# Optimization experiments

Hardware: AMD Instinct MI355X
Metric: run time of the kernel (lower is better)

## Reference

```python
import jax, jax.numpy as jnp
import numpy as np

N = 64      # SSM state size (hidden_size)
H = 1024    # channels
L = 2048    # sequence length
BATCH = 8


def setup_inputs() -> dict:
    key = jax.random.key(0)
    ks = jax.random.split(key, 12)
    s = 1.0 / np.sqrt(N)
    n = jnp.arange(N, dtype=jnp.float32)
    return {
        "r": jax.random.normal(ks[0], (BATCH, L, H), dtype=jnp.float32),
        "B_re": jax.random.normal(ks[1], (N,), dtype=jnp.float32) * s,
        "B_im": jax.random.normal(ks[2], (N,), dtype=jnp.float32) * s,
        "C_re": jax.random.normal(ks[3], (H, N), dtype=jnp.float32) * s,
        "C_im": jax.random.normal(ks[4], (H, N), dtype=jnp.float32) * s,
        "P_re": jax.random.normal(ks[5], (N,), dtype=jnp.float32) * s,
        "P_im": jax.random.normal(ks[6], (N,), dtype=jnp.float32) * s,
        "Q_re": jax.random.normal(ks[7], (N,), dtype=jnp.float32) * s,
        "Q_im": jax.random.normal(ks[8], (N,), dtype=jnp.float32) * s,
        # HiPPO-LegS-like diagonal: negative real part for stability, imag ~ pi*n
        "diag_re": -0.5 * jnp.ones((N,), dtype=jnp.float32),
        "diag_im": jnp.pi * (n - N / 2.0),
        "step": jnp.array([1e-3], dtype=jnp.float32),
        "D": jnp.zeros((1,), dtype=jnp.float32),
    }


def _dplr_kernel(Bc, Cc, Pc, Qc, Lam, step, seq_len):
    # Standard S4 DPLR generating function evaluated at roots of unity,
    # then inverse FFT -> real convolution kernel K_c of shape (H, L).
    z = jnp.exp(-2j * jnp.pi * jnp.arange(seq_len) / seq_len).astype(jnp.complex64)  # (L,)
    g = (2.0 / step) * (1.0 - z) / (1.0 + z)                                          # (L,)
    cden = 1.0 / (g[:, None] - Lam[None, :])                                          # (L,N) Cauchy denom
    k00 = jnp.einsum('hn,ln->hl', Cc * Bc, cden)   # (H,L)
    k01 = jnp.einsum('hn,ln->hl', Cc * Pc, cden)   # (H,L)
    k10 = jnp.einsum('n,ln->l', Qc * Bc, cden)     # (L,)
    k11 = jnp.einsum('n,ln->l', Qc * Pc, cden)     # (L,)
    at_roots = (2.0 / (1.0 + z)) * (k00 - k01 * (k10 / (1.0 + k11)))  # (H,L)
    return jnp.fft.ifft(at_roots, axis=-1).real


def reference(r, B_re, B_im, C_re, C_im, P_re, P_im, Q_re, Q_im,
              diag_re, diag_im, step, D):
    step_c = jnp.maximum(step[0], 1e-6)
    Bc = B_re + 1j * B_im
    Cc = C_re + 1j * C_im
    Pc = P_re + 1j * P_im
    Qc = Q_re + 1j * Q_im
    Lam = diag_re + 1j * diag_im
    seq_len = r.shape[1]
    K = _dplr_kernel(Bc, Cc, Pc, Qc, Lam, step_c, seq_len)  # (H, L)
    # causal FFT convolution along the sequence axis
    nfft = 2 * seq_len
    Kf = jnp.fft.rfft(K, n=nfft, axis=-1)            # (H, nfft//2+1)
    uf = jnp.fft.rfft(r, n=nfft, axis=1)             # (B, nfft//2+1, H)
    h1 = jnp.fft.irfft(uf * Kf.T[None], n=nfft, axis=1)[:, :seq_len]  # (B,L,H)
    y1 = h1 + D[0] * r
    return jax.nn.gelu(y1, approximate=False)
```

## Files before the change

kernel.cpp:

```cpp
#include <hip/hip_runtime.h>
#include <math.h>

#define SSM_N 64
#define SSM_H 1024
#define SSM_L 2048
#define SSM_B 8
#define FFTN 2048
#define NT 256

#define PSWZ(a) ((a) ^ (((a) >> 4) & 15))

typedef float f2 __attribute__((ext_vector_type(2)));
static __device__ __forceinline__ f2 mkf2(float a, float b){ f2 v; v.x = a; v.y = b; return v; }

static __device__ __forceinline__ f2 cmul(f2 a, f2 b){
  return mkf2(-a.y, a.y) * mkf2(b.y, b.x) + mkf2(a.x, a.x) * b;
}
static __device__ __forceinline__ f2 cconj(f2 a){ return mkf2(a.x, -a.y); }

template<bool INV> static __device__ __forceinline__ f2 mul_mi(f2 a){
  return INV ? mkf2(-a.y, a.x) : mkf2(a.y, -a.x);
}
template<bool INV> static __device__ __forceinline__ f2 mul_w81(f2 a){
  const float r = 0.70710678118654752440f;
  return INV ? (r * mkf2(a.x - a.y, a.y + a.x)) : (r * mkf2(a.x + a.y, a.y - a.x));
}
template<bool INV> static __device__ __forceinline__ f2 mul_w83(f2 a){
  const float r = 0.70710678118654752440f;
  return INV ? (r * mkf2(-(a.x + a.y), a.x - a.y)) : (r * mkf2(a.y - a.x, -(a.x + a.y)));
}

#define W8C0 1.f
#define W8S0 0.f
#define W8C1 0.92387953251f
#define W8S1 (-0.38268343236f)
#define W8C2 0.70710678119f
#define W8S2 (-0.70710678119f)
#define W8C3 0.38268343236f
#define W8S3 (-0.92387953251f)
#define W8C4 0.f
#define W8S4 (-1.f)
#define W8C5 (-0.38268343236f)
#define W8S5 (-0.92387953251f)
#define W8C6 (-0.70710678119f)
#define W8S6 (-0.70710678119f)
#define W8C7 (-0.92387953251f)
#define W8S7 (-0.38268343236f)

template<bool INV>
static __device__ __forceinline__ void bfly8_store(f2* __restrict__ dst, const f2* __restrict__ tw,
                                                   f2* x, int j, int base, int S)
{
  f2 t0=x[0]+x[4], t4=x[0]-x[4];
  f2 t1=x[1]+x[5], t5=x[1]-x[5];
  f2 t2=x[2]+x[6], t6=x[2]-x[6];
  f2 t3=x[3]+x[7], t7=x[3]-x[7];
  f2 b0=t0+t2, b2=t0-t2, b1=t1+t3, b3=t1-t3;
  f2 mb3 = mul_mi<INV>(b3);
  f2 y0=b0+b1, y4=b0-b1, y2=b2+mb3, y6=b2-mb3;
  f2 v1 = mul_w81<INV>(t5), v2 = mul_mi<INV>(t6), v3 = mul_w83<INV>(t7);
  f2 a0=t4+v2, a2=t4-v2, a1=v1+v3, a3=v1-v3;
  f2 ma3 = mul_mi<INV>(a3);
  f2 y1=a0+a1, y5=a0-a1, y3=a2+ma3, y7=a2-ma3;
  f2 w1 = tw[j];
  if (INV) w1.y = -w1.y;
  f2 w2 = cmul(w1,w1);
  f2 w3 = cmul(w2,w1);
  f2 w4 = cmul(w2,w2);
  f2 w5 = cmul(w3,w2);
  f2 w6 = cmul(w3,w3);
  f2 w7 = cmul(w4,w3);
  dst[PSWZ(base)]     = y0;
  dst[PSWZ(base+S)]   = cmul(y1,w1);
  dst[PSWZ(base+2*S)] = cmul(y2,w2);
  dst[PSWZ(base+3*S)] = cmul(y3,w3);
  dst[PSWZ(base+4*S)] = cmul(y4,w4);
  dst[PSWZ(base+5*S)] = cmul(y5,w5);
  dst[PSWZ(base+6*S)] = cmul(y6,w6);
  dst[PSWZ(base+7*S)] = cmul(y7,w7);
}

template<bool INV, bool ZTOP>
static __device__ __forceinline__ void stage8_first(const f2* __restrict__ src, f2* __restrict__ dst,
                                                    const f2* __restrict__ tw, int t, int st)
{
  const f2* sp = src + st;
  f2 x[8];
  if (ZTOP) {
    #pragma unroll
    for (int q = 0; q < 4; ++q) { x[q] = sp[256*q]; x[q+4] = mkf2(0.f, 0.f); }
  } else {
    #pragma unroll
    for (int q = 0; q < 8; ++q) x[q] = sp[256*q];
  }
  bfly8_store<INV>(dst, tw, x, t, t*8, 1);
}

template<bool INV, int S>
static __device__ __forceinline__ void stage8_mid(const f2* __restrict__ src, f2* __restrict__ dst,
                                                  const f2* __restrict__ tw, int t, int st)
{
  const f2* sp = src + st;
  f2 x[8];
  #pragma unroll
  for (int q = 0; q < 8; ++q) x[q] = sp[256*q];
  int i = t & (S-1);
  int j = t - i;
  bfly8_store<INV>(dst, tw, x, j, i + j*8, S);
}

template<bool INV, bool HALFOUT>
static __device__ __forceinline__ void stage4f(const f2* __restrict__ src, f2* __restrict__ dst, int st)
{
  #pragma unroll
  for (int hh = 0; hh < 2; ++hh) {
    const f2* sp = src + st + 256*hh;
    f2* wp = dst + st + 256*hh;
    f2 x0=sp[0], x1=sp[512], x2=sp[1024], x3=sp[1536];
    f2 a0=x0+x2, a2=x0-x2, a1=x1+x3, a3=x1-x3;
    f2 m = mul_mi<INV>(a3);
    wp[0]   = a0+a1;
    wp[512] = a2+m;
    if (!HALFOUT) {
      wp[1024] = a0-a1;
      wp[1536] = a2-m;
    }
  }
}

template<bool INV, bool ZTOP, bool HALFOUT>
static __device__ void fft2048(f2* A, f2* B, const f2* tw, int t, int st)
{
  __syncthreads();
  stage8_first<INV, ZTOP>(A, B, tw, t, st);
  __syncthreads();
  stage8_mid<INV, 8>(B, A, tw, t, st);
  __syncthreads();
  stage8_mid<INV, 64>(A, B, tw, t, st);
  __syncthreads();
  stage4f<INV, HALFOUT>(B, A, st);
  __syncthreads();
}

static __device__ __forceinline__ void init_tw(f2* tw, int t)
{
  float s, c;
  sincosf(-6.2831853071795864769f * (float)t / (float)FFTN, &s, &c);
  tw[t] = mkf2(c, s);
}

__global__ __launch_bounds__(256) void kprep(
    const float* __restrict__ r, float* __restrict__ rT,
    const float* __restrict__ B_re, const float* __restrict__ B_im,
    const float* __restrict__ P_re, const float* __restrict__ P_im,
    const float* __restrict__ Q_re, const float* __restrict__ Q_im,
    const float* __restrict__ diag_re, const float* __restrict__ diag_im,
    const float* __restrict__ step,
    f2* __restrict__ cdenT, f2* __restrict__ f2v, f2* __restrict__ facv)
{
  __shared__ float til[64][65];
  int bid = blockIdx.x;
  int t = threadIdx.x;
  if (bid < 4096) {
    int tx = t & 15, ty = t >> 4;
    int h0 = (bid & 15) * 64, l0 = ((bid >> 4) & 31) * 64, b = bid >> 9;
    const float4* s4 = (const float4*)(r + ((size_t)b*SSM_L + l0)*SSM_H + h0);
    #pragma unroll
    for (int i = 0; i < 4; ++i) {
      int lr = ty + 16*i;
      float4 v = s4[(size_t)lr*(SSM_H/4) + tx];
      til[lr][4*tx+0]=v.x; til[lr][4*tx+1]=v.y; til[lr][4*tx+2]=v.z; til[lr][4*tx+3]=v.w;
    }
    __syncthreads();
    float4* d4 = (float4*)(rT + ((size_t)b*SSM_H + h0)*SSM_L + l0);
    #pragma unroll
    for (int i = 0; i < 4; ++i) {
      int hr = ty + 16*i;
      float4 w;
      w.x = til[4*tx+0][hr]; w.y = til[4*tx+1][hr];
      w.z = til[4*tx+2][hr]; w.w = til[4*tx+3][hr];
      d4[(size_t)hr*(SSM_L/4) + tx] = w;
    }
  } else {
    int gid = (bid - 4096) * 256 + t;
    int l = gid >> 3, s = gid & 7;
    double stepc = (double)step[0]; if (stepc < 1e-6) stepc = 1e-6;
    double ang = -2.0 * 3.14159265358979323846 * (double)l / (double)SSM_L;
    double zr = cos(ang), zi = sin(ang);
    double dr = 1.0 + zr, di = zi;
    double nr = 1.0 - zr, ni = -zi;
    double den = dr*dr + di*di;
    double i2s = 2.0 / stepc;
    double gr = i2s * (nr*dr + ni*di) / den;
    double gi = i2s * (ni*dr - nr*di) / den;
    double k10r=0.0, k10i=0.0, k11r=0.0, k11i=0.0;
    #pragma unroll
    for (int q = 0; q < 8; ++q) {
      int n = s*8 + q;
      double ar = gr - (double)diag_re[n];
      double ai = gi - (double)diag_im[n];
      double d2 = ar*ar + ai*ai;
      double cr = ar/d2, ci = -ai/d2;
      cdenT[n*SSM_L + l] = mkf2((float)cr, (float)ci);
      double qr = (double)Q_re[n], qi = (double)Q_im[n];
      double br = (double)B_re[n], bi = (double)B_im[n];
      double pr = (double)P_re[n], pi = (double)P_im[n];
      double qbr = qr*br - qi*bi, qbi = qr*bi + qi*br;
      double qpr = qr*pr - qi*pi, qpi = qr*pi + qi*pr;
      k10r += qbr*cr - qbi*ci; k10i += qbr*ci + qbi*cr;
      k11r += qpr*cr - qpi*ci; k11i += qpr*ci + qpi*cr;
    }
    #pragma unroll
    for (int off = 1; off < 8; off <<= 1) {
      k10r += __shfl_xor(k10r, off);
      k10i += __shfl_xor(k10i, off);
      k11r += __shfl_xor(k11r, off);
      k11i += __shfl_xor(k11i, off);
    }
    if (s == 0) {
      f2v[l] = mkf2((float)(2.0*dr/den), (float)(-2.0*di/den));
      double er = 1.0 + k11r, ei = k11i;
      double ed = er*er + ei*ei;
      facv[l] = mkf2((float)((k10r*er + k10i*ei)/ed), (float)((k10i*er - k10r*ei)/ed));
    }
  }
}

__global__ __launch_bounds__(NT, 2) void kkern(
    const float* __restrict__ C_re, const float* __restrict__ C_im,
    const float* __restrict__ B_re, const float* __restrict__ B_im,
    const float* __restrict__ P_re, const float* __restrict__ P_im,
    const f2* __restrict__ cdenT, const f2* __restrict__ f2v, const f2* __restrict__ facv,
    float4* __restrict__ PQg)
{
  __shared__ f2 bufA[FFTN];
  __shared__ f2 bufB[FFTN];
  __shared__ f2 tw[256];
  int t = threadIdx.x, st = PSWZ(t);
  int h0 = blockIdx.x * 2;
  init_tw(tw, t);
  f2* cbs = bufA;
  if (t < 128) {
    int h = h0 + (t >> 6), n = t & 63;
    f2 cc = mkf2(C_re[h*SSM_N + n], C_im[h*SSM_N + n]);
    cbs[t]       = cmul(cc, mkf2(B_re[n], B_im[n]));
    cbs[128 + t] = cmul(cc, mkf2(P_re[n], P_im[n]));
  }
  __syncthreads();
  f2 k00[2][8], k01[2][8];
  #pragma unroll
  for (int h = 0; h < 2; ++h)
    #pragma unroll
    for (int i = 0; i < 8; ++i) { k00[h][i] = mkf2(0.f,0.f); k01[h][i] = mkf2(0.f,0.f); }
  f2 cd[8];
  #pragma unroll
  for (int i = 0; i < 8; ++i) cd[i] = cdenT[t + i*NT];
  for (int n = 0; n < SSM_N; ++n) {
    f2 cdn[8];
    #pragma unroll
    for (int i = 0; i < 8; ++i) cdn[i] = cdenT[((n+1)&63)*SSM_L + t + i*NT];
    #pragma unroll
    for (int h = 0; h < 2; ++h) {
      f2 cb = cbs[h*64 + n], cp = cbs[128 + h*64 + n];
      #pragma unroll
      for (int i = 0; i < 8; ++i) {
        k00[h][i] = k00[h][i] + cmul(cb, cd[i]);
        k01[h][i] = k01[h][i] + cmul(cp, cd[i]);
      }
    }
    #pragma unroll
    for (int i = 0; i < 8; ++i) cd[i] = cdn[i];
  }
  const float Wc8[8] = {W8C0,W8C1,W8C2,W8C3,W8C4,W8C5,W8C6,W8C7};
  const float Ws8[8] = {W8S0,W8S1,W8S2,W8S3,W8S4,W8S5,W8S6,W8S7};
  float sb, cb2;
  sincosf(-3.14159265358979f * (float)t / (float)FFTN, &sb, &cb2);
  f2 cbase = mkf2(cb2, sb);
  for (int hh = 0; hh < 2; ++hh) {
    __syncthreads();
    #pragma unroll
    for (int i = 0; i < 8; ++i) {
      int l = t + i*NT;
      f2 fv = f2v[l], fc = facv[l];
      bufA[PSWZ(l)] = cmul(fv, k00[hh][i] - cmul(k01[hh][i], fc));
    }
    __syncthreads();
    f2 ebin[4]; f2 e2048 = mkf2(0.f, 0.f);
    #pragma unroll
    for (int i = 0; i < 4; ++i) {
      int m = t + i*NT;
      if (m == 0) {
        ebin[i] = mkf2(bufA[0].x, 0.f);
        e2048   = mkf2(bufA[PSWZ(FFTN/2)].x, 0.f);
      } else {
        ebin[i] = 0.5f * (bufA[PSWZ(m)] + cconj(bufA[PSWZ(FFTN - m)]));
      }
    }
    fft2048<true, false, false>(bufA, bufB, tw, t, st);
    const float scale = 1.0f / (float)FFTN;
    #pragma unroll
    for (int i = 0; i < 8; ++i) {
      int n = t + i*NT;
      float K = bufA[PSWZ(n)].x * scale;
      bufA[PSWZ(n)] = K * cmul(cbase, mkf2(Wc8[i], Ws8[i]));
    }
    fft2048<false, false, true>(bufA, bufB, tw, t, st);
    #pragma unroll
    for (int i = 0; i < 4; ++i) bufB[t + i*NT] = ebin[i];
    if (t == 0) bufB[FFTN/2] = e2048;
    __syncthreads();
    float4* pqrow = PQg + (size_t)(h0 + hh) * FFTN;
    const float q4 = 1.0f / 4096.0f;
    #pragma unroll
    for (int i = 0; i < 4; ++i) {
      int m = t + i*NT;
      f2 Ka = bufB[m];
      f2 Kb = bufB[1024 - m];
      float sv, cv;
      sincosf(3.0679615757712824e-3f * (float)m, &sv, &cv);
      float am = q4*(1.f - sv), ap = q4*(1.f + sv), cq = q4*cv;
      f2 P = mkf2(Ka.x*am + Kb.x*ap, Ka.y*am - Kb.y*ap);
      f2 dd = mkf2(Ka.x - Kb.x, Ka.y + Kb.y);
      pqrow[2*m] = make_float4(P.x, P.y, -dd.y*cq, dd.x*cq);
    }
    #pragma unroll
    for (int i = 0; i < 4; ++i) {
      int m = t + i*NT;
      f2 Ka = bufA[PSWZ(m)];
      f2 Kb = bufA[PSWZ(1023 - m)];
      float sv, cv;
      sincosf(1.5339807878856412e-3f * (float)(2*m+1), &sv, &cv);
      float am = q4*(1.f - sv), ap = q4*(1.f + sv), cq = q4*cv;
      f2 P = mkf2(Ka.x*am + Kb.x*ap, Ka.y*am - Kb.y*ap);
      f2 dd = mkf2(Ka.x - Kb.x, Ka.y + Kb.y);
      pqrow[2*m+1] = make_float4(P.x, P.y, -dd.y*cq, dd.x*cq);
    }
  }
}

__global__ __launch_bounds__(NT, 4) void kconv(float* __restrict__ rT,
                                               const float4* __restrict__ PQg,
                                               const float* __restrict__ Dp)
{
  __shared__ f2 bufA[FFTN];
  __shared__ f2 bufB[FFTN];
  __shared__ f2 tw[256];
  int t = threadIdx.x, st = PSWZ(t);
  int xc = blockIdx.x & 7, y = blockIdx.x >> 3;
  int h = xc * 128 + (y >> 3);
  int b = y & 7;
  float Dv = Dp[0];
  init_tw(tw, t);
  float* rrow = rT + ((size_t)b*SSM_H + h) * SSM_L;
  const f2* r2 = (const f2*)rrow;
  f2 rv[4];
  #pragma unroll
  for (int i = 0; i < 4; ++i) rv[i] = r2[t + i*NT];
  {
    f2 xx[8];
    #pragma unroll
    for (int q = 0; q < 4; ++q) { xx[q] = rv[q]; xx[q+4] = mkf2(0.f, 0.f); }
    bfly8_store<false>(bufB, tw, xx, t, t*8, 1);
  }
  __syncthreads();
  stage8_mid<false, 8>(bufB, bufA, tw, t, st);
  __syncthreads();
  stage8_mid<false, 64>(bufA, bufB, tw, t, st);
  __syncthreads();
  const float4* pqrow = PQg + (size_t)h * FFTN;
  float4 pq[8];
  #pragma unroll
  for (int i = 0; i < 8; ++i) pq[i] = pqrow[t + i*NT];
  stage4f<false, false>(bufB, bufA, st);
  __syncthreads();
  {
    f2 xx[8];
    #pragma unroll
    for (int i = 0; i < 8; ++i) {
      int k = t + i*NT;
      int kk = (FFTN - k) & (FFTN - 1);
      f2 Ck  = bufA[st + i*NT];
      f2 Ckk = bufA[PSWZ(kk)];
      xx[i] = cmul(mkf2(pq[i].x, pq[i].y), Ck) + cmul(mkf2(pq[i].z, pq[i].w), cconj(Ckk));
    }
    bfly8_store<true>(bufB, tw, xx, t, t*8, 1);
  }
  __syncthreads();
  stage8_mid<true, 8>(bufB, bufA, tw, t, st);
  __syncthreads();
  stage8_mid<true, 64>(bufA, bufB, tw, t, st);
  __syncthreads();
  f2* o2 = (f2*)rrow;
  #pragma unroll
  for (int hh = 0; hh < 2; ++hh) {
    const f2* sp = bufB + st + 256*hh;
    f2 x0=sp[0], x1=sp[512], x2=sp[1024], x3=sp[1536];
    f2 a0=x0+x2, a2=x0-x2, a1=x1+x3, a3=x1-x3;
    f2 mm = mul_mi<true>(a3);
    f2 y0 = a0+a1, y1 = a2+mm;
    f2 rA = rv[hh], rB = rv[hh+2];
    o2[t + 256*hh]       = mkf2(y0.x + Dv*rA.x, y0.y + Dv*rA.y);
    o2[t + 256*hh + 512] = mkf2(y1.x + Dv*rB.x, y1.y + Dv*rB.y);
  }
}

__global__ __launch_bounds__(256) void ktback(const float* __restrict__ yT, float* __restrict__ out)
{
  __shared__ float til[64][65];
  int t = threadIdx.x, tx = t & 15, ty = t >> 4;
  int h0 = blockIdx.x * 64, l0 = blockIdx.y * 64, b = blockIdx.z;
  const float4* s4 = (const float4*)(yT + ((size_t)b*SSM_H + h0)*SSM_L + l0);
  #pragma unroll
  for (int i = 0; i < 4; ++i) {
    int hr = ty + 16*i;
    float4 v = s4[(size_t)hr*(SSM_L/4) + tx];
    til[hr][4*tx+0]=v.x; til[hr][4*tx+1]=v.y; til[hr][4*tx+2]=v.z; til[hr][4*tx+3]=v.w;
  }
  __syncthreads();
  float4* d4 = (float4*)(out + ((size_t)b*SSM_L + l0)*SSM_H + h0);
  #pragma unroll
  for (int i = 0; i < 4; ++i) {
    int lr = ty + 16*i;
    float4 w;
    float x0 = til[4*tx+0][lr], x1 = til[4*tx+1][lr];
    float x2 = til[4*tx+2][lr], x3 = til[4*tx+3][lr];
    w.x = 0.5f * x0 * (1.0f + erff(x0 * 0.70710678118654752f));
    w.y = 0.5f * x1 * (1.0f + erff(x1 * 0.70710678118654752f));
    w.z = 0.5f * x2 * (1.0f + erff(x2 * 0.70710678118654752f));
    w.w = 0.5f * x3 * (1.0f + erff(x3 * 0.70710678118654752f));
    d4[(size_t)lr*(SSM_H/4) + tx] = w;
  }
}

extern "C" void kernel_launch(void* const* d_in, const int* in_sizes, int n_in,
                              void* d_out, int out_size, void* d_ws, size_t ws_size,
                              hipStream_t stream)
{
  const float* r       = (const float*)d_in[0];
  const float* B_re    = (const float*)d_in[1];
  const float* B_im    = (const float*)d_in[2];
  const float* C_re    = (const float*)d_in[3];
  const float* C_im    = (const float*)d_in[4];
  const float* P_re    = (const float*)d_in[5];
  const float* P_im    = (const float*)d_in[6];
  const float* Q_re    = (const float*)d_in[7];
  const float* Q_im    = (const float*)d_in[8];
  const float* diag_re = (const float*)d_in[9];
  const float* diag_im = (const float*)d_in[10];
  const float* step    = (const float*)d_in[11];
  const float* Dp      = (const float*)d_in[12];
  float* out = (float*)d_out;

  char* p = (char*)d_ws;
  float* rT  = (float*)p;  p += (size_t)SSM_B*SSM_H*SSM_L*sizeof(float);
  f2* cdenT  = (f2*)p;     p += (size_t)SSM_N*SSM_L*sizeof(f2);
  f2* f2v    = (f2*)p;     p += (size_t)SSM_L*sizeof(f2);
  f2* facv   = (f2*)p;     p += (size_t)SSM_L*sizeof(f2);
  float4* PQ = (float4*)p; p += (size_t)SSM_H*FFTN*sizeof(float4);

  kprep<<<4096 + 64, 256, 0, stream>>>(r, rT, B_re, B_im, P_re, P_im, Q_re, Q_im,
                                       diag_re, diag_im, step, cdenT, f2v, facv);
  kkern<<<SSM_H/2, NT, 0, stream>>>(C_re, C_im, B_re, B_im, P_re, P_im,
                                    cdenT, f2v, facv, PQ);
  kconv<<<SSM_B*SSM_H, NT, 0, stream>>>(rT, PQ, Dp);
  ktback<<<dim3(SSM_H/64, SSM_L/64, SSM_B), 256, 0, stream>>>(rT, out);
}
```

Measured before the change: 267.0 us.

## Batch both channels' FFTs in kkern, keep first/last stages in registers

```diff
diff --git a/kernel.cpp b/kernel.cpp
--- a/kernel.cpp
+++ b/kernel.cpp
@@ -48,8 +48,7 @@
 #define W8S7 (-0.38268343236f)
 
 template<bool INV>
-static __device__ __forceinline__ void bfly8_store(f2* __restrict__ dst, const f2* __restrict__ tw,
-                                                   f2* x, int j, int base, int S)
+static __device__ __forceinline__ void bfly8(const f2* x, f2* y)
 {
   f2 t0=x[0]+x[4], t4=x[0]-x[4];
   f2 t1=x[1]+x[5], t5=x[1]-x[5];
@@ -57,43 +56,42 @@
   f2 t3=x[3]+x[7], t7=x[3]-x[7];
   f2 b0=t0+t2, b2=t0-t2, b1=t1+t3, b3=t1-t3;
   f2 mb3 = mul_mi<INV>(b3);
-  f2 y0=b0+b1, y4=b0-b1, y2=b2+mb3, y6=b2-mb3;
+  y[0]=b0+b1; y[4]=b0-b1; y[2]=b2+mb3; y[6]=b2-mb3;
   f2 v1 = mul_w81<INV>(t5), v2 = mul_mi<INV>(t6), v3 = mul_w83<INV>(t7);
   f2 a0=t4+v2, a2=t4-v2, a1=v1+v3, a3=v1-v3;
   f2 ma3 = mul_mi<INV>(a3);
-  f2 y1=a0+a1, y5=a0-a1, y3=a2+ma3, y7=a2-ma3;
+  y[1]=a0+a1; y[5]=a0-a1; y[3]=a2+ma3; y[7]=a2-ma3;
+}
+
+template<bool INV>
+static __device__ __forceinline__ void calc_w8(const f2* __restrict__ tw, int j, f2* w)
+{
   f2 w1 = tw[j];
   if (INV) w1.y = -w1.y;
-  f2 w2 = cmul(w1,w1);
-  f2 w3 = cmul(w2,w1);
-  f2 w4 = cmul(w2,w2);
-  f2 w5 = cmul(w3,w2);
-  f2 w6 = cmul(w3,w3);
-  f2 w7 = cmul(w4,w3);
-  dst[PSWZ(base)]     = y0;
-  dst[PSWZ(base+S)]   = cmul(y1,w1);
-  dst[PSWZ(base+2*S)] = cmul(y2,w2);
-  dst[PSWZ(base+3*S)] = cmul(y3,w3);
-  dst[PSWZ(base+4*S)] = cmul(y4,w4);
-  dst[PSWZ(base+5*S)] = cmul(y5,w5);
-  dst[PSWZ(base+6*S)] = cmul(y6,w6);
-  dst[PSWZ(base+7*S)] = cmul(y7,w7);
-}
-
-template<bool INV, bool ZTOP>
-static __device__ __forceinline__ void stage8_first(const f2* __restrict__ src, f2* __restrict__ dst,
-                                                    const f2* __restrict__ tw, int t, int st)
-{
-  const f2* sp = src + st;
-  f2 x[8];
-  if (ZTOP) {
-    #pragma unroll
-    for (int q = 0; q < 4; ++q) { x[q] = sp[256*q]; x[q+4] = mkf2(0.f, 0.f); }
-  } else {
-    #pragma unroll
-    for (int q = 0; q < 8; ++q) x[q] = sp[256*q];
-  }
-  bfly8_store<INV>(dst, tw, x, t, t*8, 1);
+  w[1]=w1; w[2]=cmul(w1,w1); w[3]=cmul(w[2],w1); w[4]=cmul(w[2],w[2]);
+  w[5]=cmul(w[3],w[2]); w[6]=cmul(w[3],w[3]); w[7]=cmul(w[4],w[3]);
+}
+
+static __device__ __forceinline__ void twstore(f2* __restrict__ dst, const f2* y, const f2* w,
+                                               int base, int S)
+{
+  dst[PSWZ(base)]     = y[0];
+  dst[PSWZ(base+S)]   = cmul(y[1],w[1]);
+  dst[PSWZ(base+2*S)] = cmul(y[2],w[2]);
+  dst[PSWZ(base+3*S)] = cmul(y[3],w[3]);
+  dst[PSWZ(base+4*S)] = cmul(y[4],w[4]);
+  dst[PSWZ(base+5*S)] = cmul(y[5],w[5]);
+  dst[PSWZ(base+6*S)] = cmul(y[6],w[6]);
+  dst[PSWZ(base+7*S)] = cmul(y[7],w[7]);
+}
+
+template<bool INV>
+static __device__ __forceinline__ void bfly8_store(f2* __restrict__ dst, const f2* __restrict__ tw,
+                                                   f2* x, int j, int base, int S)
+{
+  f2 y[8]; bfly8<INV>(x, y);
+  f2 w[8]; calc_w8<INV>(tw, j, w);
+  twstore(dst, y, w, base, S);
 }
 
 template<bool INV, int S>
@@ -107,6 +105,23 @@
   int i = t & (S-1);
   int j = t - i;
   bfly8_store<INV>(dst, tw, x, j, i + j*8, S);
+}
+
+template<bool INV, int S>
+static __device__ __forceinline__ void stage8_mid2(const f2* __restrict__ s0, f2* __restrict__ d0,
+                                                   const f2* __restrict__ s1, f2* __restrict__ d1,
+                                                   const f2* __restrict__ tw, int t, int st)
+{
+  f2 x0[8], x1[8];
+  #pragma unroll
+  for (int q = 0; q < 8; ++q) x0[q] = s0[st + 256*q];
+  #pragma unroll
+  for (int q = 0; q < 8; ++q) x1[q] = s1[st + 256*q];
+  int i = t & (S-1), j = t - i, base = i + j*8;
+  f2 w[8]; calc_w8<INV>(tw, j, w);
+  f2 y[8];
+  bfly8<INV>(x0, y); twstore(d0, y, w, base, S);
+  bfly8<INV>(x1, y); twstore(d1, y, w, base, S);
 }
 
 template<bool INV, bool HALFOUT>
@@ -128,25 +143,29 @@
   }
 }
 
-template<bool INV, bool ZTOP, bool HALFOUT>
-static __device__ void fft2048(f2* A, f2* B, const f2* tw, int t, int st)
-{
-  __syncthreads();
-  stage8_first<INV, ZTOP>(A, B, tw, t, st);
-  __syncthreads();
-  stage8_mid<INV, 8>(B, A, tw, t, st);
-  __syncthreads();
-  stage8_mid<INV, 64>(A, B, tw, t, st);
-  __syncthreads();
-  stage4f<INV, HALFOUT>(B, A, st);
-  __syncthreads();
-}
-
-static __device__ __forceinline__ void init_tw(f2* tw, int t)
+template<bool INV>
+static __device__ __forceinline__ void stage4f_reg(const f2* __restrict__ src, f2* out, int st)
+{
+  #pragma unroll
+  for (int hh = 0; hh < 2; ++hh) {
+    const f2* sp = src + st + 256*hh;
+    f2 x0=sp[0], x1=sp[512], x2=sp[1024], x3=sp[1536];
+    f2 a0=x0+x2, a2=x0-x2, a1=x1+x3, a3=x1-x3;
+    f2 m = mul_mi<INV>(a3);
+    out[hh]   = a0+a1;
+    out[hh+2] = a2+m;
+    out[hh+4] = a0-a1;
+    out[hh+6] = a2-m;
+  }
+}
+
+static __device__ __forceinline__ f2 init_tw(f2* tw, int t)
 {
   float s, c;
   sincosf(-6.2831853071795864769f * (float)t / (float)FFTN, &s, &c);
-  tw[t] = mkf2(c, s);
+  f2 v = mkf2(c, s);
+  tw[t] = v;
+  return v;
 }
 
 __global__ __launch_bounds__(256) void kprep(
@@ -233,13 +252,13 @@
     const f2* __restrict__ cdenT, const f2* __restrict__ f2v, const f2* __restrict__ facv,
     float4* __restrict__ PQg)
 {
-  __shared__ f2 bufA[FFTN];
-  __shared__ f2 bufB[FFTN];
+  __shared__ f2 bufA[2][FFTN];
+  __shared__ f2 bufB[2][FFTN];
   __shared__ f2 tw[256];
   int t = threadIdx.x, st = PSWZ(t);
   int h0 = blockIdx.x * 2;
-  init_tw(tw, t);
-  f2* cbs = bufA;
+  f2 u = init_tw(tw, t);
+  f2* cbs = bufA[0];
   if (t < 128) {
     int h = h0 + (t >> 6), n = t & 63;
     f2 cc = mkf2(C_re[h*SSM_N + n], C_im[h*SSM_N + n]);
@@ -271,69 +290,109 @@
     #pragma unroll
     for (int i = 0; i < 8; ++i) cd[i] = cdn[i];
   }
-  const float Wc8[8] = {W8C0,W8C1,W8C2,W8C3,W8C4,W8C5,W8C6,W8C7};
-  const float Ws8[8] = {W8S0,W8S1,W8S2,W8S3,W8S4,W8S5,W8S6,W8S7};
   float sb, cb2;
   sincosf(-3.14159265358979f * (float)t / (float)FFTN, &sb, &cb2);
   f2 cbase = mkf2(cb2, sb);
-  for (int hh = 0; hh < 2; ++hh) {
-    __syncthreads();
+  __syncthreads();
+  f2 ar[2][8];
+  #pragma unroll
+  for (int hh = 0; hh < 2; ++hh)
     #pragma unroll
     for (int i = 0; i < 8; ++i) {
       int l = t + i*NT;
       f2 fv = f2v[l], fc = facv[l];
-      bufA[PSWZ(l)] = cmul(fv, k00[hh][i] - cmul(k01[hh][i], fc));
-    }
-    __syncthreads();
-    f2 ebin[4]; f2 e2048 = mkf2(0.f, 0.f);
+      ar[hh][i] = cmul(fv, k00[hh][i] - cmul(k01[hh][i], fc));
+      bufA[hh][PSWZ(l)] = ar[hh][i];
+    }
+  __syncthreads();
+  f2 ebin[2][4], e2048[2];
+  e2048[0] = mkf2(0.f,0.f); e2048[1] = mkf2(0.f,0.f);
+  #pragma unroll
+  for (int ch = 0; ch < 2; ++ch) {
     #pragma unroll
     for (int i = 0; i < 4; ++i) {
       int m = t + i*NT;
       if (m == 0) {
-        ebin[i] = mkf2(bufA[0].x, 0.f);
-        e2048   = mkf2(bufA[PSWZ(FFTN/2)].x, 0.f);
+        ebin[ch][0] = mkf2(bufA[ch][0].x, 0.f);
+        e2048[ch]   = mkf2(bufA[ch][PSWZ(FFTN/2)].x, 0.f);
       } else {
-        ebin[i] = 0.5f * (bufA[PSWZ(m)] + cconj(bufA[PSWZ(FFTN - m)]));
+        ebin[ch][i] = 0.5f * (bufA[ch][PSWZ(m)] + cconj(bufA[ch][PSWZ(FFTN - m)]));
       }
     }
-    fft2048<true, false, false>(bufA, bufB, tw, t, st);
+  }
+  {
+    f2 w[8]; calc_w8<true>(tw, t, w);
+    f2 y[8];
+    bfly8<true>(ar[0], y); twstore(bufB[0], y, w, t*8, 1);
+    bfly8<true>(ar[1], y); twstore(bufB[1], y, w, t*8, 1);
+  }
+  __syncthreads();
+  stage8_mid2<true, 8>(bufB[0], bufA[0], bufB[1], bufA[1], tw, t, st);
+  __syncthreads();
+  stage8_mid2<true, 64>(bufA[0], bufB[0], bufA[1], bufB[1], tw, t, st);
+  __syncthreads();
+  {
+    f2 kr0[8], kr1[8];
+    stage4f_reg<true>(bufB[0], kr0, st);
+    stage4f_reg<true>(bufB[1], kr1, st);
+    const float Wc8[8] = {W8C0,W8C1,W8C2,W8C3,W8C4,W8C5,W8C6,W8C7};
+    const float Ws8[8] = {W8S0,W8S1,W8S2,W8S3,W8S4,W8S5,W8S6,W8S7};
     const float scale = 1.0f / (float)FFTN;
     #pragma unroll
-    for (int i = 0; i < 8; ++i) {
-      int n = t + i*NT;
-      float K = bufA[PSWZ(n)].x * scale;
-      bufA[PSWZ(n)] = K * cmul(cbase, mkf2(Wc8[i], Ws8[i]));
-    }
-    fft2048<false, false, true>(bufA, bufB, tw, t, st);
-    #pragma unroll
-    for (int i = 0; i < 4; ++i) bufB[t + i*NT] = ebin[i];
-    if (t == 0) bufB[FFTN/2] = e2048;
-    __syncthreads();
-    float4* pqrow = PQg + (size_t)(h0 + hh) * FFTN;
-    const float q4 = 1.0f / 4096.0f;
+    for (int q = 0; q < 8; ++q) {
+      f2 tq = cmul(cbase, mkf2(Wc8[q], Ws8[q]));
+      kr0[q] = (kr0[q].x * scale) * tq;
+      kr1[q] = (kr1[q].x * scale) * tq;
+    }
+    f2 w[8]; calc_w8<false>(tw, t, w);
+    f2 y[8];
+    bfly8<false>(kr0, y); twstore(bufA[0], y, w, t*8, 1);
+    bfly8<false>(kr1, y); twstore(bufA[1], y, w, t*8, 1);
+  }
+  __syncthreads();
+  stage8_mid2<false, 8>(bufA[0], bufB[0], bufA[1], bufB[1], tw, t, st);
+  __syncthreads();
+  stage8_mid2<false, 64>(bufB[0], bufA[0], bufB[1], bufA[1], tw, t, st);
+  __syncthreads();
+  #pragma unroll
+  for (int ch = 0; ch < 2; ++ch) {
+    stage4f<false, true>(bufA[ch], bufB[ch], st);
     #pragma unroll
     for (int i = 0; i < 4; ++i) {
       int m = t + i*NT;
-      f2 Ka = bufB[m];
-      f2 Kb = bufB[1024 - m];
-      float sv, cv;
-      sincosf(3.0679615757712824e-3f * (float)m, &sv, &cv);
+      f2 v = ebin[ch][i];
+      if (m == 0) v = e2048[ch];
+      bufB[ch][1024 + m] = v;
+    }
+  }
+  __syncthreads();
+  const float q4 = 1.0f / 4096.0f;
+  const f2 c1 = mkf2(0.99999882345170176f, -0.00153398018628477f);
+  f2 base_odd = cmul(c1, u);
+  const float Wc8[8] = {W8C0,W8C1,W8C2,W8C3,W8C4,W8C5,W8C6,W8C7};
+  const float Ws8[8] = {W8S0,W8S1,W8S2,W8S3,W8S4,W8S5,W8S6,W8S7};
+  #pragma unroll
+  for (int ch = 0; ch < 2; ++ch) {
+    float4* pqrow = PQg + (size_t)(h0 + ch) * FFTN;
+    #pragma unroll
+    for (int i = 0; i < 4; ++i) {
+      int m = t + i*NT;
+      f2 Ka = ebin[ch][i];
+      f2 Kb = bufB[ch][1024 + ((1024 - m) & 1023)];
+      f2 ee = cmul(u, mkf2(Wc8[2*i], Ws8[2*i]));
+      float cv = ee.x, sv = -ee.y;
       float am = q4*(1.f - sv), ap = q4*(1.f + sv), cq = q4*cv;
       f2 P = mkf2(Ka.x*am + Kb.x*ap, Ka.y*am - Kb.y*ap);
       f2 dd = mkf2(Ka.x - Kb.x, Ka.y + Kb.y);
       pqrow[2*m] = make_float4(P.x, P.y, -dd.y*cq, dd.x*cq);
-    }
-    #pragma unroll
-    for (int i = 0; i < 4; ++i) {
-      int m = t + i*NT;
-      f2 Ka = bufA[PSWZ(m)];
-      f2 Kb = bufA[PSWZ(1023 - m)];
-      float sv, cv;
-      sincosf(1.5339807878856412e-3f * (float)(2*m+1), &sv, &cv);
-      float am = q4*(1.f - sv), ap = q4*(1.f + sv), cq = q4*cv;
-      f2 P = mkf2(Ka.x*am + Kb.x*ap, Ka.y*am - Kb.y*ap);
-      f2 dd = mkf2(Ka.x - Kb.x, Ka.y + Kb.y);
-      pqrow[2*m+1] = make_float4(P.x, P.y, -dd.y*cq, dd.x*cq);
+      f2 Ko = bufB[ch][PSWZ(m)];
+      f2 Kp = bufB[ch][PSWZ(1023 - m)];
+      f2 eo = cmul(base_odd, mkf2(Wc8[2*i], Ws8[2*i]));
+      cv = eo.x; sv = -eo.y;
+      am = q4*(1.f - sv); ap = q4*(1.f + sv); cq = q4*cv;
+      f2 P2 = mkf2(Ko.x*am + Kp.x*ap, Ko.y*am - Kp.y*ap);
+      f2 d2 = mkf2(Ko.x - Kp.x, Ko.y + Kp.y);
+      pqrow[2*m+1] = make_float4(P2.x, P2.y, -d2.y*cq, d2.x*cq);
     }
   }
 }
```

Result: no change. 265.3 us (-0.6%).
